# Performance work log

Hardware: AMD Instinct MI355X
Metric: run time of the kernel (lower is better)

Reference implementation:

```python
import jax, jax.numpy as jnp
import numpy as np
from jax import lax

E = 8          # num_experts
K = 2          # top-k
TASKS = 8
GATE_DIM = 16
# (in, expand, out, kernel, stride) per MoE stage
STAGES = [(3, 32, 16, 7, 2), (16, 64, 32, 3, 1), (32, 128, 64, 3, 2), (64, 256, 64, 3, 1), (64, 128, 32, 3, 1)]
DN = ('NCHW', 'OIHW', 'NCHW')


def _pw(x, w):
    return lax.conv_general_dilated(x, w, (1, 1), 'VALID', dimension_numbers=DN)


def _dw(x, w, s):
    p = w.shape[-1] // 2
    return lax.conv_general_dilated(x, w, (s, s), [(p, p), (p, p)], dimension_numbers=DN, feature_group_count=x.shape[1])


def _gn(x, scale, bias):
    # GroupNorm with num_groups = C // 4, eps = 1e-5 (torch default)
    B, C, H, W = x.shape
    G = C // 4
    xr = x.reshape(B, G, -1)
    m = xr.mean(-1, keepdims=True)
    v = xr.var(-1, keepdims=True)
    xn = ((xr - m) * lax.rsqrt(v + 1e-5)).reshape(B, C, H, W)
    return xn * scale[None, :, None, None] + bias[None, :, None, None]


def _dsc(x, p, stride):
    # DSCBlock: pw-conv -> GN -> SiLU -> dw-conv -> GN -> SiLU -> pw-conv -> GN
    w1, s1, b1, w2, s2, b2, w3, s3, b3 = p
    x = jax.nn.silu(_gn(_pw(x, w1), s1, b1))
    x = jax.nn.silu(_gn(_dw(x, w2, stride), s2, b2))
    return _gn(_pw(x, w3), s3, b3)


def _moe(gate_input, x, wg, p, stride, task_bh):
    # task-conditioned top-k softmax gating (noisy_gating=False, all aux loss weights 0)
    logits = gate_input @ wg[task_bh]                      # (B, E)
    probs = jax.nn.softmax(logits, axis=-1)
    topv, topi = lax.top_k(probs, K)
    topv = topv / topv.sum(-1, keepdims=True)              # renormalize top-k gates
    Bn = gate_input.shape[0]
    dense = jnp.zeros_like(probs).at[jnp.arange(Bn)[:, None], topi].set(topv)
    eo = jax.vmap(lambda pe: _dsc(x, pe, stride))(p)       # (E, B, C, H, W)
    return jnp.einsum('be,ebchw->bchw', dense, eo)


def _forward(fl, task_bh):
    gi, xi, ppe = fl[0], fl[1], fl[2]
    x = xi
    for i, (_, _, _, _, s) in enumerate(STAGES):
        base = 3 + i * 10
        wg = fl[base]
        p = tuple(fl[base + 1: base + 10])
        x = _moe(gi, x, wg, p, s, task_bh)
    Bn = x.shape[0]
    # patchify: (B,32,20,20) -> unfold(2,4,4).unfold(3,4,4) -> permute -> (B,25,512)
    patches = x.reshape(Bn, 32, 5, 4, 5, 4).transpose(0, 1, 2, 4, 3, 5)  # (B,32,5,5,4,4)
    patches = patches.transpose(0, 2, 3, 4, 5, 1).reshape(Bn, 25, 512)
    return patches + ppe


def setup_inputs():
    key = jax.random.key(0)
    ks = iter(jax.random.split(key, 256))
    B = 64
    d = {}
    d['gate_input'] = jax.random.normal(next(ks), (B, GATE_DIM), jnp.float32)
    d['expert_input'] = jax.random.normal(next(ks), (B, 3, 80, 80), jnp.float32)
    d['patch_pos_embed'] = 0.02 * jax.random.normal(next(ks), (1, 25, 512), jnp.float32)
    for i, (cin, exp, cout, k, s) in enumerate(STAGES, 1):
        d[f's{i}_wg'] = 0.1 * jax.random.normal(next(ks), (TASKS, GATE_DIM, E), jnp.float32)
        d[f's{i}_w1'] = jax.random.normal(next(ks), (E, exp, cin, 1, 1), jnp.float32) / np.sqrt(cin)
        d[f's{i}_g1s'] = 1.0 + 0.1 * jax.random.normal(next(ks), (E, exp), jnp.float32)
        d[f's{i}_g1b'] = 0.1 * jax.random.normal(next(ks), (E, exp), jnp.float32)
        d[f's{i}_w2'] = jax.random.normal(next(ks), (E, exp, 1, k, k), jnp.float32) / k
        d[f's{i}_g2s'] = 1.0 + 0.1 * jax.random.normal(next(ks), (E, exp), jnp.float32)
        d[f's{i}_g2b'] = 0.1 * jax.random.normal(next(ks), (E, exp), jnp.float32)
        d[f's{i}_w3'] = jax.random.normal(next(ks), (E, cout, exp, 1, 1), jnp.float32) / np.sqrt(exp)
        d[f's{i}_g3s'] = 1.0 + 0.1 * jax.random.normal(next(ks), (E, cout), jnp.float32)
        d[f's{i}_g3b'] = 0.1 * jax.random.normal(next(ks), (E, cout), jnp.float32)
    d['task_bh'] = 3
    return d


def reference(gate_input, expert_input, patch_pos_embed, s1_wg, s1_w1, s1_g1s, s1_g1b, s1_w2, s1_g2s, s1_g2b, s1_w3, s1_g3s, s1_g3b, s2_wg, s2_w1, s2_g1s, s2_g1b, s2_w2, s2_g2s, s2_g2b, s2_w3, s2_g3s, s2_g3b, s3_wg, s3_w1, s3_g1s, s3_g1b, s3_w2, s3_g2s, s3_g2b, s3_w3, s3_g3s, s3_g3b, s4_wg, s4_w1, s4_g1s, s4_g1b, s4_w2, s4_g2s, s4_g2b, s4_w3, s4_g3s, s4_g3b, s5_wg, s5_w1, s5_g1s, s5_g1b, s5_w2, s5_g2s, s5_g2b, s5_w3, s5_g3s, s5_g3b, task_bh):
    fl = (gate_input, expert_input, patch_pos_embed,
          s1_wg, s1_w1, s1_g1s, s1_g1b, s1_w2, s1_g2s, s1_g2b, s1_w3, s1_g3s, s1_g3b,
          s2_wg, s2_w1, s2_g1s, s2_g1b, s2_w2, s2_g2s, s2_g2b, s2_w3, s2_g3s, s2_g3b,
          s3_wg, s3_w1, s3_g1s, s3_g1b, s3_w2, s3_g2s, s3_g2b, s3_w3, s3_g3s, s3_g3b,
          s4_wg, s4_w1, s4_g1s, s4_g1b, s4_w2, s4_g2s, s4_g2b, s4_w3, s4_g3s, s4_g3b,
          s5_wg, s5_w1, s5_g1s, s5_g1b, s5_w2, s5_g2s, s5_g2b, s5_w3, s5_g3s, s5_g3b)
    patches = _forward(fl, task_bh)
    loss = jnp.zeros((), patches.dtype)  # all MoE loss weights are 0 in VisionEncoder
    return (patches, loss)
```

## Files before the change

kernel.cpp:

```cpp
#include <hip/hip_runtime.h>
#include <cstddef>

#define TPB 256

__device__ __forceinline__ int rfl(int v) { return __builtin_amdgcn_readfirstlane(v); }
__device__ __forceinline__ float rflf(float v) {
    return __int_as_float(__builtin_amdgcn_readfirstlane(__float_as_int(v)));
}

__device__ __forceinline__ unsigned short f2bf(float f) {
    union { float f; unsigned int u; } x{f};
    unsigned int r = x.u + 0x7fffu + ((x.u >> 16) & 1u);
    return (unsigned short)(r >> 16);
}
__device__ __forceinline__ float bf2f(unsigned short u) {
    return __uint_as_float(((unsigned int)u) << 16);
}

template <int N, int NW>
__device__ __forceinline__ void bredN(float* v, float* red) {
    __syncthreads();
    #pragma unroll
    for (int off = 32; off > 0; off >>= 1)
        #pragma unroll
        for (int i = 0; i < N; i++) v[i] += __shfl_down(v[i], off);
    const int lane = threadIdx.x & 63;
    const int wv = threadIdx.x >> 6;
    if (lane == 0)
        #pragma unroll
        for (int i = 0; i < N; i++) red[wv * N + i] = v[i];
    __syncthreads();
    if (threadIdx.x == 0) {
        #pragma unroll
        for (int i = 0; i < N; i++) {
            float s = 0.f;
            #pragma unroll
            for (int w = 0; w < NW; w++) s += red[w * N + i];
            red[i] = s;
        }
    }
    __syncthreads();
    #pragma unroll
    for (int i = 0; i < N; i++) v[i] = red[i];
}

__device__ __forceinline__ float silu_f(float v) {
    return v * __builtin_amdgcn_rcpf(1.f + __expf(-v));
}

struct GatePtrs { const float* wg[5]; };

__global__ void gate_kernel(const float* __restrict__ gi, GatePtrs gp,
                            const int* __restrict__ taskp,
                            int* __restrict__ gidx, float* __restrict__ gw) {
    const int s = blockIdx.x;
    const int b = threadIdx.x;
    const int task = taskp[0];
    const float* wg = gp.wg[s] + (size_t)task * 16 * 8;
    float l[8];
    #pragma unroll
    for (int e = 0; e < 8; e++) l[e] = 0.f;
    for (int d = 0; d < 16; d++) {
        float v = gi[b * 16 + d];
        #pragma unroll
        for (int e = 0; e < 8; e++) l[e] += v * wg[d * 8 + e];
    }
    float mx = l[0];
    #pragma unroll
    for (int e = 1; e < 8; e++) mx = fmaxf(mx, l[e]);
    float p[8]; float sum = 0.f;
    #pragma unroll
    for (int e = 0; e < 8; e++) { p[e] = expf(l[e] - mx); sum += p[e]; }
    int i0 = 0;
    #pragma unroll
    for (int e = 1; e < 8; e++) if (p[e] > p[i0]) i0 = e;
    int i1 = (i0 == 0) ? 1 : 0;
    #pragma unroll
    for (int e = 0; e < 8; e++) if (e != i0 && p[e] > p[i1]) i1 = e;
    const float denom = p[i0] + p[i1];
    const int base = (s * 64 + b) * 2;
    gidx[base] = i0; gidx[base + 1] = i1;
    gw[base] = p[i0] / denom; gw[base + 1] = p[i1] / denom;
}

__global__ __launch_bounds__(256) void s1_stats(
    const float* __restrict__ xin, const float* __restrict__ w1,
    const int* __restrict__ gidx, float* __restrict__ stats1) {
    const int g = blockIdx.x, b = blockIdx.y, slot = blockIdx.z;
    const int tid = threadIdx.x;
    const int e = rfl(gidx[b * 2 + slot]);
    __shared__ float red[8];
    const float* xb = xin + (size_t)b * 3 * 6400;
    const float* w1e = w1 + ((size_t)e * 32 + g * 4) * 3;
    float wr[4][3];
    #pragma unroll
    for (int c = 0; c < 4; c++)
        #pragma unroll
        for (int k = 0; k < 3; k++) wr[c][k] = rflf(w1e[c * 3 + k]);
    float s[2] = {0.f, 0.f};
    #pragma unroll
    for (int j = 0; j < 7; j++) {
        const int i = j * 256 + tid;
        if (i < 1600) {
            const int p4 = i * 4;
            const float4 v0 = *(const float4*)(xb + p4);
            const float4 v1 = *(const float4*)(xb + 6400 + p4);
            const float4 v2 = *(const float4*)(xb + 12800 + p4);
            const float a0[4] = {v0.x, v0.y, v0.z, v0.w};
            const float a1[4] = {v1.x, v1.y, v1.z, v1.w};
            const float a2[4] = {v2.x, v2.y, v2.z, v2.w};
            #pragma unroll
            for (int t = 0; t < 4; t++)
                #pragma unroll
                for (int c = 0; c < 4; c++) {
                    float a = fmaf(wr[c][0], a0[t], fmaf(wr[c][1], a1[t], wr[c][2] * a2[t]));
                    s[0] += a; s[1] += a * a;
                }
        }
    }
    bredN<2, 4>(s, red);
    if (tid == 0) {
        float* sp = stats1 + ((size_t)(b * 2 + slot) * 8 + g) * 2;
        sp[0] = s[0]; sp[1] = s[1];
    }
}

__global__ __launch_bounds__(256) void s1_band(
    const float* __restrict__ xin, const float* __restrict__ w1,
    const float* __restrict__ g1s, const float* __restrict__ g1b,
    const float* __restrict__ w2, const int* __restrict__ gidx,
    const float* __restrict__ stats1,
    float* __restrict__ rawdw, float* __restrict__ stats2) {
    constexpr int NR = 25, RW = 90, EVO = 44;
    const int gb = blockIdx.x;
    const int g = gb >> 2, band = gb & 3;
    const int b = blockIdx.y, slot = blockIdx.z;
    const int tid = threadIdx.x;
    const int e = rfl(gidx[b * 2 + slot]);

    __shared__ float sbuf[4 * NR * RW];
    __shared__ float w2s[196];
    __shared__ float red[8];

    for (int i = tid; i < 4 * NR * RW; i += 256) sbuf[i] = 0.f;
    if (tid < 196) w2s[tid] = w2[((size_t)e * 32 + g * 4) * 49 + tid];

    const float* sp = stats1 + ((size_t)(b * 2 + slot) * 8 + g) * 2;
    const float s1v = rflf(sp[0]), s2v = rflf(sp[1]);
    const float mean = s1v / 25600.f;
    const float var = s2v / 25600.f - mean * mean;
    const float inv = rsqrtf(var + 1e-5f);

    const float* xb = xin + (size_t)b * 3 * 6400;
    const float* w1e = w1 + ((size_t)e * 32 + g * 4) * 3;
    float wr[4][3], sc1r[4], bi1r[4];
    #pragma unroll
    for (int c = 0; c < 4; c++) {
        #pragma unroll
        for (int k = 0; k < 3; k++) wr[c][k] = rflf(w1e[c * 3 + k]);
        sc1r[c] = rflf(g1s[e * 32 + g * 4 + c]);
        bi1r[c] = rflf(g1b[e * 32 + g * 4 + c]);
    }
    const int oh0 = band * 10;
    const int rlo = 2 * oh0 - 3;
    __syncthreads();

    for (int ii = tid; ii < 500; ii += 256) {
        const int p4 = ii * 4;
        const int l = p4 / 80, pw = p4 - l * 80;
        const int r = rlo + l;
        if (r >= 0 && r < 80) {
            const float4 v0 = *(const float4*)(xb + r * 80 + pw);
            const float4 v1 = *(const float4*)(xb + 6400 + r * 80 + pw);
            const float4 v2 = *(const float4*)(xb + 12800 + r * 80 + pw);
            const float a0[4] = {v0.x, v0.y, v0.z, v0.w};
            const float a1[4] = {v1.x, v1.y, v1.z, v1.w};
            const float a2[4] = {v2.x, v2.y, v2.z, v2.w};
            #pragma unroll
            for (int c = 0; c < 4; c++) {
                #pragma unroll
                for (int t = 0; t < 4; t++) {
                    float a = fmaf(wr[c][0], a0[t], fmaf(wr[c][1], a1[t], wr[c][2] * a2[t]));
                    float v = silu_f((a - mean) * inv * sc1r[c] + bi1r[c]);
                    const int cc = pw + t + 3;
                    const int sl = (cc & 1) ? EVO + (cc >> 1) : (cc >> 1);
                    sbuf[(c * NR + l) * RW + sl] = v;
                }
            }
        }
    }
    __syncthreads();

    float st2[2] = {0.f, 0.f};
    float* rw = rawdw + (size_t)(b * 2 + slot) * 32 * 1600 + (size_t)g * 4 * 1600;
    #pragma unroll
    for (int qi = 0; qi < 2; qi++) {
        const int q = tid + qi * 256;
        if (q < 400) {
            const int c = q / 100;
            const int rem = q - c * 100;
            const int ohl = rem / 10, owb = (rem - ohl * 10) * 4;
            float o[4] = {0.f, 0.f, 0.f, 0.f};
            #pragma unroll
            for (int kh = 0; kh < 7; kh++) {
                const int base = (c * NR + 2 * ohl + kh) * RW;
                const float2 e01 = *(const float2*)&sbuf[base + owb];
                const float2 e23 = *(const float2*)&sbuf[base + owb + 2];
                const float2 e45 = *(const float2*)&sbuf[base + owb + 4];
                const float e6 = sbuf[base + owb + 6];
                const float2 q01 = *(const float2*)&sbuf[base + EVO + owb];
                const float2 q23 = *(const float2*)&sbuf[base + EVO + owb + 2];
                const float2 q45 = *(const float2*)&sbuf[base + EVO + owb + 4];
                const float evr[7] = {e01.x, e01.y, e23.x, e23.y, e45.x, e45.y, e6};
                const float odr[6] = {q01.x, q01.y, q23.x, q23.y, q45.x, q45.y};
                const float w0 = w2s[c * 49 + kh * 7 + 0];
                const float w1v = w2s[c * 49 + kh * 7 + 1];
                const float w2v = w2s[c * 49 + kh * 7 + 2];
                const float w3 = w2s[c * 49 + kh * 7 + 3];
                const float w4 = w2s[c * 49 + kh * 7 + 4];
                const float w5 = w2s[c * 49 + kh * 7 + 5];
                const float w6 = w2s[c * 49 + kh * 7 + 6];
                #pragma unroll
                for (int t = 0; t < 4; t++)
                    o[t] += w0 * evr[t] + w1v * odr[t] + w2v * evr[t + 1]
                          + w3 * odr[t + 1] + w4 * evr[t + 2] + w5 * odr[t + 2]
                          + w6 * evr[t + 3];
            }
            const int oh = oh0 + ohl;
            float4 ov = {o[0], o[1], o[2], o[3]};
            *(float4*)(rw + c * 1600 + oh * 40 + owb) = ov;
            #pragma unroll
            for (int t = 0; t < 4; t++) { st2[0] += o[t]; st2[1] += o[t] * o[t]; }
        }
    }
    bredN<2, 4>(st2, red);
    if (tid == 0) {
        float* s2p = stats2 + (((size_t)(b * 2 + slot) * 8 + g) * 4 + band) * 2;
        s2p[0] = st2[0]; s2p[1] = st2[1];
    }
}

__global__ __launch_bounds__(256) void s1_norm(
    const float* __restrict__ rawdw, const float* __restrict__ stats2,
    const float* __restrict__ g2s, const float* __restrict__ g2b,
    const int* __restrict__ gidx, unsigned short* __restrict__ act2) {
    const int g = blockIdx.x, b = blockIdx.y, slot = blockIdx.z;
    const int tid = threadIdx.x;
    const int e = rfl(gidx[b * 2 + slot]);
    const float* sp = stats2 + ((size_t)(b * 2 + slot) * 8 + g) * 8;
    const float s1 = rflf(sp[0]) + rflf(sp[2]) + rflf(sp[4]) + rflf(sp[6]);
    const float s2 = rflf(sp[1]) + rflf(sp[3]) + rflf(sp[5]) + rflf(sp[7]);
    const float mean2 = s1 / 6400.f;
    const float var2 = s2 / 6400.f - mean2 * mean2;
    const float inv2 = rsqrtf(var2 + 1e-5f);
    const float* rb = rawdw + (size_t)(b * 2 + slot) * 32 * 1600 + (size_t)g * 4 * 1600;
    unsigned short* ao = act2 + ((size_t)(b * 2 + slot) * 32 + g * 4) * 1600;
    #pragma unroll
    for (int c = 0; c < 4; c++) {
        const float sc = rflf(g2s[e * 32 + g * 4 + c]);
        const float bi = rflf(g2b[e * 32 + g * 4 + c]);
        #pragma unroll
        for (int qi = 0; qi < 2; qi++) {
            const int i = tid + qi * 256;
            if (i < 400) {
                const float4 v = *(const float4*)(rb + c * 1600 + i * 4);
                ushort4 ov;
                ov.x = f2bf(silu_f((v.x - mean2) * inv2 * sc + bi));
                ov.y = f2bf(silu_f((v.y - mean2) * inv2 * sc + bi));
                ov.z = f2bf(silu_f((v.z - mean2) * inv2 * sc + bi));
                ov.w = f2bf(silu_f((v.w - mean2) * inv2 * sc + bi));
                *(ushort4*)(ao + c * 1600 + i * 4) = ov;
            }
        }
    }
}

template <int CIN, int CEXP, int KS, int STRIDE, int H, int W, int HO, int WO,
          int NCH, int TPBk>
__global__ __launch_bounds__(TPBk) void dsc_ab_v2(
    const unsigned short* __restrict__ xin, const float* __restrict__ w1,
    const float* __restrict__ g1s, const float* __restrict__ g1b,
    const float* __restrict__ w2,
    const float* __restrict__ g2s, const float* __restrict__ g2b,
    const int* __restrict__ gidx, unsigned short* __restrict__ act2) {
    constexpr int HW = H * W, HWO = HO * WO;
    constexpr int HP = H + 2, WPL = W + 3, EVW = (W + 2) / 2;
    constexpr int NPV = HW / 4;
    constexpr int JN = (NPV + TPBk - 1) / TPBk;
    constexpr int NW = TPBk / 64;
    constexpr int NG = NCH / 4;
    constexpr int Qc = HWO / 4;
    constexpr int QT = NCH * Qc;
    constexpr int QI = (QT + TPBk - 1) / TPBk;
    constexpr int KK = KS * KS;
    const int gch = blockIdx.x, b = blockIdx.y, slot = blockIdx.z;
    const int tid = threadIdx.x;
    const int e = rfl(gidx[b * 2 + slot]);
    const int cb0 = gch * NCH;

    __shared__ float buf1[NCH * HP * WPL];
    __shared__ float w2s[NCH * KK];
    __shared__ float sc2s[NCH], bi2s[NCH];
    __shared__ float red[2 * NG * NW];

    for (int i = tid; i < NCH * HP * WPL; i += TPBk) buf1[i] = 0.f;
    for (int i = tid; i < NCH * KK; i += TPBk) {
        int c = i / KK, k = i - c * KK;
        w2s[i] = w2[((size_t)e * CEXP + cb0 + c) * KK + k];
    }
    if (tid < NCH) {
        sc2s[tid] = g2s[e * CEXP + cb0 + tid];
        bi2s[tid] = g2b[e * CEXP + cb0 + tid];
    }

    const unsigned short* xb = xin + (size_t)b * CIN * HW;
    const float* w1e = w1 + ((size_t)e * CEXP + cb0) * CIN;

    float acc[NCH][JN][4];
    #pragma unroll
    for (int c = 0; c < NCH; c++)
        #pragma unroll
        for (int j = 0; j < JN; j++)
            #pragma unroll
            for (int t = 0; t < 4; t++) acc[c][j][t] = 0.f;

    for (int cb = 0; cb < CIN; cb += 4) {
        float wr[NCH][4];
        #pragma unroll
        for (int c = 0; c < NCH; c++)
            #pragma unroll
            for (int k = 0; k < 4; k++) wr[c][k] = rflf(w1e[c * CIN + cb + k]);
        #pragma unroll
        for (int j = 0; j < JN; j++) {
            const int pv = tid + j * TPBk;
            if (JN * TPBk == NPV || pv < NPV) {
                #pragma unroll
                for (int k = 0; k < 4; k++) {
                    const ushort4 v4 = *(const ushort4*)(xb + (cb + k) * HW + pv * 4);
                    const float va[4] = {bf2f(v4.x), bf2f(v4.y), bf2f(v4.z), bf2f(v4.w)};
                    #pragma unroll
                    for (int c = 0; c < NCH; c++)
                        #pragma unroll
                        for (int t = 0; t < 4; t++)
                            acc[c][j][t] = fmaf(wr[c][k], va[t], acc[c][j][t]);
                }
            }
        }
    }
    float st[2 * NG];
    #pragma unroll
    for (int i = 0; i < 2 * NG; i++) st[i] = 0.f;
    #pragma unroll
    for (int c = 0; c < NCH; c++) {
        const int gs = (c >> 2) * 2;
        #pragma unroll
        for (int j = 0; j < JN; j++)
            #pragma unroll
            for (int t = 0; t < 4; t++) {
                float a = acc[c][j][t];
                st[gs] += a; st[gs + 1] += a * a;
            }
    }
    bredN<2 * NG, NW>(st, red);
    float mg[NG], ig[NG];
    #pragma unroll
    for (int g = 0; g < NG; g++) {
        mg[g] = st[g * 2] / (4.f * HW);
        float var = st[g * 2 + 1] / (4.f * HW) - mg[g] * mg[g];
        ig[g] = rsqrtf(var + 1e-5f);
    }
    float sc1r[NCH], bi1r[NCH];
    #pragma unroll
    for (int c = 0; c < NCH; c++) {
        sc1r[c] = rflf(g1s[e * CEXP + cb0 + c]);
        bi1r[c] = rflf(g1b[e * CEXP + cb0 + c]);
    }
    #pragma unroll
    for (int j = 0; j < JN; j++) {
        const int pv = tid + j * TPBk;
        if (JN * TPBk == NPV || pv < NPV) {
            const int p4 = pv * 4;
            const int ph = p4 / W, pwb = p4 - ph * W;
            #pragma unroll
            for (int c = 0; c < NCH; c++) {
                const int g = (NG == 1) ? 0 : (c >> 2);
                #pragma unroll
                for (int t = 0; t < 4; t++) {
                    float v = silu_f((acc[c][j][t] - mg[g]) * ig[g] * sc1r[c] + bi1r[c]);
                    const int j2 = pwb + t + 1;
                    const int col = (STRIDE == 1) ? j2
                                    : ((j2 & 1) ? EVW + (j2 >> 1) : (j2 >> 1));
                    buf1[(c * HP + ph + 1) * WPL + col] = v;
                }
            }
        }
    }
    __syncthreads();

    float dacc[QI][4];
    float st2[2 * NG];
    #pragma unroll
    for (int i = 0; i < 2 * NG; i++) st2[i] = 0.f;
    #pragma unroll
    for (int qi = 0; qi < QI; qi++) {
        #pragma unroll
        for (int t = 0; t < 4; t++) dacc[qi][t] = 0.f;
        const int q = tid + qi * TPBk;
        if (QI * TPBk == QT || q < QT) {
            const int c = q / Qc, qq = q - c * Qc;
            const int oh = qq % HO, owb = (qq / HO) * 4;
            float o[4] = {0.f, 0.f, 0.f, 0.f};
            if (STRIDE == 1) {
                #pragma unroll
                for (int kh = 0; kh < KS; kh++) {
                    const int base = (c * HP + oh + kh) * WPL + owb;
                    float r[6];
                    #pragma unroll
                    for (int i = 0; i < 6; i++) r[i] = buf1[base + i];
                    const float wa = w2s[c * KK + kh * KS + 0];
                    const float wb = w2s[c * KK + kh * KS + 1];
                    const float wcc = w2s[c * KK + kh * KS + 2];
                    #pragma unroll
                    for (int t = 0; t < 4; t++)
                        o[t] += wa * r[t] + wb * r[t + 1] + wcc * r[t + 2];
                }
            } else {
                #pragma unroll
                for (int kh = 0; kh < KS; kh++) {
                    const int base = (c * HP + 2 * oh + kh) * WPL;
                    float ev[5], od[4];
                    #pragma unroll
                    for (int i = 0; i < 5; i++) ev[i] = buf1[base + owb + i];
                    #pragma unroll
                    for (int i = 0; i < 4; i++) od[i] = buf1[base + EVW + owb + i];
                    const float wa = w2s[c * KK + kh * KS + 0];
                    const float wb = w2s[c * KK + kh * KS + 1];
                    const float wcc = w2s[c * KK + kh * KS + 2];
                    #pragma unroll
                    for (int t = 0; t < 4; t++)
                        o[t] += wa * ev[t] + wb * od[t] + wcc * ev[t + 1];
                }
            }
            #pragma unroll
            for (int t = 0; t < 4; t++) {
                float a = o[t];
                dacc[qi][t] = a;
                if constexpr (NG == 1) {
                    st2[0] += a; st2[1] += a * a;
                } else {
                    const bool gsel = (c >= 4);
                    float a0 = gsel ? 0.f : a, a1 = gsel ? a : 0.f;
                    st2[0] += a0; st2[1] += a0 * a0;
                    st2[2] += a1; st2[3] += a1 * a1;
                }
            }
        }
    }
    bredN<2 * NG, NW>(st2, red);
    float m2[NG], i2[NG];
    #pragma unroll
    for (int g = 0; g < NG; g++) {
        m2[g] = st2[g * 2] / (4.f * HWO);
        float var = st2[g * 2 + 1] / (4.f * HWO) - m2[g] * m2[g];
        i2[g] = rsqrtf(var + 1e-5f);
    }
    unsigned short* ao = act2 + ((size_t)(b * 2 + slot) * CEXP + cb0) * HWO;
    #pragma unroll
    for (int qi = 0; qi < QI; qi++) {
        const int q = tid + qi * TPBk;
        if (QI * TPBk == QT || q < QT) {
            const int c = q / Qc, qq = q - c * Qc;
            const int oh = qq % HO, owb = (qq / HO) * 4;
            const int g = (NG == 1) ? 0 : ((c >= 4) ? 1 : 0);
            const float sc = sc2s[c], bi = bi2s[c];
            ushort4 ov;
            ov.x = f2bf(silu_f((dacc[qi][0] - m2[g]) * i2[g] * sc + bi));
            ov.y = f2bf(silu_f((dacc[qi][1] - m2[g]) * i2[g] * sc + bi));
            ov.z = f2bf(silu_f((dacc[qi][2] - m2[g]) * i2[g] * sc + bi));
            ov.w = f2bf(silu_f((dacc[qi][3] - m2[g]) * i2[g] * sc + bi));
            *(ushort4*)(ao + c * HWO + oh * WO + owb) = ov;
        }
    }
}

template <int CEXP, int COUT, int HWO, int MT, int NT, int VEC, int PXC>
__global__ __launch_bounds__(256) void pw3_k1(
    const unsigned short* __restrict__ act2, const float* __restrict__ w3,
    const int* __restrict__ gidx,
    float* __restrict__ raw3, float* __restrict__ statsw) {
    constexpr int NTILE = NT * VEC;
    static_assert(MT * NT == 256 && NTILE == 64, "tile");
    constexpr int G = COUT / 4;
    constexpr int KC = 16;
    constexpr int WPT = (KC * COUT) / 256;
    const int pxc = blockIdx.x, b = blockIdx.y, slot = blockIdx.z;
    const int tid = threadIdx.x;
    const int e = rfl(gidx[b * 2 + slot]);
    const int px0 = pxc * NTILE;
    const int ct = tid / NT, pt = tid % NT;

    __shared__ float actT[KC][NTILE];
    __shared__ float wT[KC][COUT];

    const unsigned short* ab = act2 + (size_t)(b * 2 + slot) * CEXP * HWO;
    const float* w3e = w3 + (size_t)e * COUT * CEXP;

    float acc[4][VEC];
    #pragma unroll
    for (int i = 0; i < 4; i++)
        #pragma unroll
        for (int j = 0; j < VEC; j++) acc[i][j] = 0.f;

    const int lkk = tid / 16;
    const int lp4 = (tid % 16) * 4;
    const int wc = tid / (KC / WPT);
    const int wk = (tid % (KC / WPT)) * WPT;

    for (int k0 = 0; k0 < CEXP; k0 += KC) {
        __syncthreads();
        {
            const int px = px0 + lp4;
            ushort4 v = make_ushort4(0, 0, 0, 0);
            if (px < HWO) v = *(const ushort4*)(ab + (size_t)(k0 + lkk) * HWO + px);
            float4 f = {bf2f(v.x), bf2f(v.y), bf2f(v.z), bf2f(v.w)};
            *(float4*)&actT[lkk][lp4] = f;
        }
        #pragma unroll
        for (int i = 0; i < WPT; i++)
            wT[wk + i][wc] = w3e[(size_t)wc * CEXP + k0 + wk + i];
        __syncthreads();
        #pragma unroll
        for (int kk = 0; kk < KC; kk++) {
            const float4 w4 = *(const float4*)&wT[kk][ct * 4];
            const float wf[4] = {w4.x, w4.y, w4.z, w4.w};
            float av[VEC];
            if constexpr (VEC == 4) {
                float4 a4 = *(const float4*)&actT[kk][pt * 4];
                av[0] = a4.x; av[1] = a4.y; av[2] = a4.z; av[3] = a4.w;
            } else if constexpr (VEC == 2) {
                float2 a2 = *(const float2*)&actT[kk][pt * 2];
                av[0] = a2.x; av[1] = a2.y;
            } else {
                av[0] = actT[kk][pt];
            }
            #pragma unroll
            for (int i = 0; i < 4; i++)
                #pragma unroll
                for (int j = 0; j < VEC; j++)
                    acc[i][j] = fmaf(wf[i], av[j], acc[i][j]);
        }
    }

    const int px = px0 + pt * VEC;
    float s1 = 0.f, s2 = 0.f;
    #pragma unroll
    for (int i = 0; i < 4; i++) {
        if (px < HWO) {
            float* rp = raw3 + ((size_t)(b * 2 + slot) * COUT + ct * 4 + i) * HWO + px;
            if constexpr (VEC == 4) {
                float4 v = {acc[i][0], acc[i][1], acc[i][2], acc[i][3]};
                *(float4*)rp = v;
            } else if constexpr (VEC == 2) {
                float2 v = {acc[i][0], acc[i][1]};
                *(float2*)rp = v;
            } else {
                *rp = acc[i][0];
            }
        }
        #pragma unroll
        for (int j = 0; j < VEC; j++) { s1 += acc[i][j]; s2 += acc[i][j] * acc[i][j]; }
    }
    #pragma unroll
    for (int off = NT / 2; off > 0; off >>= 1) {
        s1 += __shfl_down(s1, off);
        s2 += __shfl_down(s2, off);
    }
    if (pt == 0) {
        float* sp = statsw + (((size_t)(b * 2 + slot) * G + ct) * PXC + pxc) * 2;
        sp[0] = s1; sp[1] = s2;
    }
}

template <int COUT, int HWO, int PXC, bool PATCH>
__global__ __launch_bounds__(256) void pw3_k3m(
    const float* __restrict__ raw3, const float* __restrict__ statsw,
    const float* __restrict__ g3s, const float* __restrict__ g3b,
    const int* __restrict__ gidx, const float* __restrict__ gw,
    const float* __restrict__ ppe, float* __restrict__ outf,
    unsigned short* __restrict__ outb) {
    constexpr int G = COUT / 4;
    constexpr int Q = HWO / 4;
    const int gg = blockIdx.x, b = blockIdx.y;
    const int tid = threadIdx.x;

    float A[2][4], Bv[2][4];
    #pragma unroll
    for (int slot = 0; slot < 2; slot++) {
        const int e = rfl(gidx[b * 2 + slot]);
        const float wgt = rflf(gw[b * 2 + slot]);
        const float* sp = statsw + ((size_t)(b * 2 + slot) * G + gg) * PXC * 2;
        float s1 = 0.f, s2 = 0.f;
        for (int i = 0; i < PXC; i++) { s1 += rflf(sp[i * 2]); s2 += rflf(sp[i * 2 + 1]); }
        const float mean = s1 / (4.f * HWO);
        const float var = s2 / (4.f * HWO) - mean * mean;
        const float inv = rsqrtf(var + 1e-5f);
        #pragma unroll
        for (int i = 0; i < 4; i++) {
            const int c = gg * 4 + i;
            const float sc = rflf(g3s[e * COUT + c]);
            const float bi = rflf(g3b[e * COUT + c]);
            A[slot][i] = wgt * inv * sc;
            Bv[slot][i] = wgt * (bi - mean * inv * sc);
        }
    }

    #pragma unroll
    for (int i = 0; i < 4; i++) {
        const int c = gg * 4 + i;
        const float* r0 = raw3 + ((size_t)(b * 2 + 0) * COUT + c) * HWO;
        const float* r1 = raw3 + ((size_t)(b * 2 + 1) * COUT + c) * HWO;
        for (int q = tid; q < Q; q += 256) {
            const int p4 = q * 4;
            const float4 v0 = *(const float4*)(r0 + p4);
            const float4 v1 = *(const float4*)(r1 + p4);
            float o[4];
            o[0] = fmaf(A[0][i], v0.x, Bv[0][i]) + fmaf(A[1][i], v1.x, Bv[1][i]);
            o[1] = fmaf(A[0][i], v0.y, Bv[0][i]) + fmaf(A[1][i], v1.y, Bv[1][i]);
            o[2] = fmaf(A[0][i], v0.z, Bv[0][i]) + fmaf(A[1][i], v1.z, Bv[1][i]);
            o[3] = fmaf(A[0][i], v0.w, Bv[0][i]) + fmaf(A[1][i], v1.w, Bv[1][i]);
            if constexpr (!PATCH) {
                ushort4 ov = {f2bf(o[0]), f2bf(o[1]), f2bf(o[2]), f2bf(o[3])};
                *(ushort4*)(outb + ((size_t)b * COUT + c) * HWO + p4) = ov;
            } else {
                const int ph = p4 / 20, pw0 = p4 - ph * 20;
                const int p = (ph >> 2) * 5 + (pw0 >> 2);
                const int dbase = ((ph & 3) * 4) * 32 + c;
                float* op = outf + ((size_t)b * 25 + p) * 512;
                const float* pp = ppe + p * 512;
                #pragma unroll
                for (int jj = 0; jj < 4; jj++)
                    op[dbase + jj * 32] = o[jj] + pp[dbase + jj * 32];
            }
        }
    }
    if (PATCH && gg == 0 && b == 0 && tid == 0) outf[64 * 25 * 512] = 0.f;
}

extern "C" void kernel_launch(void* const* d_in, const int* in_sizes, int n_in,
                              void* d_out, int out_size, void* d_ws, size_t ws_size,
                              hipStream_t stream) {
    const float* gate_input = (const float*)d_in[0];
    const float* expert_input = (const float*)d_in[1];
    const float* ppe = (const float*)d_in[2];
    const int* taskp = (const int*)d_in[53];
    auto in = [&](int s, int k) { return (const float*)d_in[3 + s * 10 + k]; };

    char* ws = (char*)d_ws;
    int* gidx = (int*)ws;
    float* gw = (float*)(ws + 4096);
    size_t off = 8192;
    unsigned short* x0 = (unsigned short*)(ws + off); off += (size_t)8 << 20;
    unsigned short* x1 = (unsigned short*)(ws + off); off += (size_t)8 << 20;
    unsigned short* act2 = (unsigned short*)(ws + off); off += (size_t)27 << 20;
    float* raw3 = (float*)(ws + off); off += (size_t)27 << 20;
    float* statsw = (float*)(ws + off); off += (size_t)1 << 20;
    float* stats1 = (float*)(ws + off); off += 65536;
    float* stats2 = (float*)(ws + off);
    float* outp = (float*)d_out;

    GatePtrs gp;
    for (int s = 0; s < 5; s++) gp.wg[s] = in(s, 0);
    gate_kernel<<<5, 64, 0, stream>>>(gate_input, gp, taskp, gidx, gw);

    s1_stats<<<dim3(8, 64, 2), 256, 0, stream>>>(expert_input, in(0, 1),
                                                 gidx + 0 * 128, stats1);
    s1_band<<<dim3(32, 64, 2), 256, 0, stream>>>(
        expert_input, in(0, 1), in(0, 2), in(0, 3), in(0, 4),
        gidx + 0 * 128, stats1, raw3, stats2);
    s1_norm<<<dim3(8, 64, 2), 256, 0, stream>>>(
        raw3, stats2, in(0, 5), in(0, 6), gidx + 0 * 128, act2);
    pw3_k1<32, 16, 1600, 4, 64, 1, 25><<<dim3(25, 64, 2), 256, 0, stream>>>(
        act2, in(0, 7), gidx + 0 * 128, raw3, statsw);
    pw3_k3m<16, 1600, 25, false><<<dim3(4, 64), 256, 0, stream>>>(
        raw3, statsw, in(0, 8), in(0, 9), gidx + 0 * 128, gw + 0 * 128, ppe,
        nullptr, x0);

    dsc_ab_v2<16, 64, 3, 1, 40, 40, 40, 40, 4, 256><<<dim3(16, 64, 2), 256, 0, stream>>>(
        x0, in(1, 1), in(1, 2), in(1, 3), in(1, 4), in(1, 5), in(1, 6),
        gidx + 1 * 128, act2);
    pw3_k1<64, 32, 1600, 8, 32, 2, 25><<<dim3(25, 64, 2), 256, 0, stream>>>(
        act2, in(1, 7), gidx + 1 * 128, raw3, statsw);
    pw3_k3m<32, 1600, 25, false><<<dim3(8, 64), 256, 0, stream>>>(
        raw3, statsw, in(1, 8), in(1, 9), gidx + 1 * 128, gw + 1 * 128, ppe,
        nullptr, x1);

    dsc_ab_v2<32, 128, 3, 2, 40, 40, 20, 20, 4, 256><<<dim3(32, 64, 2), 256, 0, stream>>>(
        x1, in(2, 1), in(2, 2), in(2, 3), in(2, 4), in(2, 5), in(2, 6),
        gidx + 2 * 128, act2);
    pw3_k1<128, 64, 400, 16, 16, 4, 7><<<dim3(7, 64, 2), 256, 0, stream>>>(
        act2, in(2, 7), gidx + 2 * 128, raw3, statsw);
    pw3_k3m<64, 400, 7, false><<<dim3(16, 64), 256, 0, stream>>>(
        raw3, statsw, in(2, 8), in(2, 9), gidx + 2 * 128, gw + 2 * 128, ppe,
        nullptr, x0);

    dsc_ab_v2<64, 256, 3, 1, 20, 20, 20, 20, 8, 128><<<dim3(32, 64, 2), 128, 0, stream>>>(
        x0, in(3, 1), in(3, 2), in(3, 3), in(3, 4), in(3, 5), in(3, 6),
        gidx + 3 * 128, act2);
    pw3_k1<256, 64, 400, 16, 16, 4, 7><<<dim3(7, 64, 2), 256, 0, stream>>>(
        act2, in(3, 7), gidx + 3 * 128, raw3, statsw);
    pw3_k3m<64, 400, 7, false><<<dim3(16, 64), 256, 0, stream>>>(
        raw3, statsw, in(3, 8), in(3, 9), gidx + 3 * 128, gw + 3 * 128, ppe,
        nullptr, x1);

    dsc_ab_v2<64, 128, 3, 1, 20, 20, 20, 20, 8, 128><<<dim3(16, 64, 2), 128, 0, stream>>>(
        x1, in(4, 1), in(4, 2), in(4, 3), in(4, 4), in(4, 5), in(4, 6),
        gidx + 4 * 128, act2);
    pw3_k1<128, 32, 400, 8, 32, 2, 7><<<dim3(7, 64, 2), 256, 0, stream>>>(
        act2, in(4, 7), gidx + 4 * 128, raw3, statsw);
    pw3_k3m<32, 400, 7, true><<<dim3(8, 64), 256, 0, stream>>>(
        raw3, statsw, in(4, 8), in(4, 9), gidx + 4 * 128, gw + 4 * 128, ppe,
        outp, nullptr);
}
```

Baseline: 547.2 us.

## Replace scalar pointwise convs with bf16 MFMA GEMMs and split DSC stages

Adds a templated bf16 MFMA GEMM kernel for the pointwise convolutions. It handles the first pw conv in stages 2, 4 and 5 and the final pw conv in every stage, replacing the fp32 FMA tiled kernel. In stages 2, 4 and 5 the fused dsc_ab_v2 kernel becomes a GEMM, then a separate depthwise kernel, then a GEMM that folds GroupNorm and SiLU into its input load. The final-conv raw output is stored as bf16 instead of fp32, which cuts memory traffic but adds rounding error before normalization. The split adds kernel launches and round-trips of the expanded activations through global memory, and the weights are converted to bf16 on every tile load.

After: 523.9 us. 1.04x faster.

```diff
diff --git a/kernel.cpp b/kernel.cpp
--- a/kernel.cpp
+++ b/kernel.cpp
@@ -2,6 +2,9 @@
 #include <cstddef>
 
 #define TPB 256
+
+typedef __attribute__((ext_vector_type(8))) short short8v;
+typedef __attribute__((ext_vector_type(4))) float f32x4;
 
 __device__ __forceinline__ int rfl(int v) { return __builtin_amdgcn_readfirstlane(v); }
 __device__ __forceinline__ float rflf(float v) {
@@ -81,6 +84,254 @@
     const int base = (s * 64 + b) * 2;
     gidx[base] = i0; gidx[base + 1] = i1;
     gw[base] = p[i0] / denom; gw[base + 1] = p[i1] / denom;
+}
+
+template <int M, int K, int N, int MT, int NCHK, bool FOLD, bool BIN>
+__global__ __launch_bounds__(256) void gemm_bf16(
+    const unsigned short* __restrict__ inp, const float* __restrict__ wmat,
+    const int* __restrict__ gidx, const float* __restrict__ foldStats,
+    const float* __restrict__ foldS, const float* __restrict__ foldB,
+    unsigned short* __restrict__ outp, float* __restrict__ stats) {
+    constexpr int KITERS = (K + 31) / 32;
+    constexpr int IM = (MT == 64) ? 2 : 1;
+    constexpr int IN = (MT == 16) ? 1 : 2;
+    const int bx = blockIdx.x;
+    const int nc = bx % NCHK, mc = bx / NCHK;
+    const int b = blockIdx.y, slot = blockIdx.z;
+    const int bs = b * 2 + slot;
+    const int e = rfl(gidx[b * 2 + slot]);
+    const int n0 = nc * 64, m0 = mc * MT;
+    const int tid = threadIdx.x;
+    const int lane = tid & 63, wv = tid >> 6;
+    const int quad = lane >> 4, l15 = lane & 15;
+
+    __shared__ __align__(16) unsigned short wtile[MT * 40];
+    __shared__ unsigned int intile[16 * 65];
+    __shared__ float sred[(MT / 4) * 2];
+    __shared__ float afv[K], bfv[K];
+
+    if (tid < (MT / 4) * 2) sred[tid] = 0.f;
+    if constexpr (FOLD) {
+        for (int c = tid; c < K; c += 256) {
+            const int g = c >> 2;
+            const float s1 = foldStats[((size_t)bs * (K / 4) + g) * 2 + 0];
+            const float s2 = foldStats[((size_t)bs * (K / 4) + g) * 2 + 1];
+            const float mean = s1 / (4.f * N);
+            const float var = s2 / (4.f * N) - mean * mean;
+            const float inv = rsqrtf(var + 1e-5f);
+            const float sc = foldS[e * K + c], bi = foldB[e * K + c];
+            afv[c] = inv * sc;
+            bfv[c] = bi - mean * inv * sc;
+        }
+    }
+
+    int mbase, nbase;
+    if constexpr (MT == 64) { mbase = (wv & 1) * 32; nbase = (wv >> 1) * 32; }
+    else if constexpr (MT == 32) { mbase = (wv & 1) * 16; nbase = (wv >> 1) * 32; }
+    else { mbase = 0; nbase = wv * 16; }
+
+    f32x4 acc[IM][IN];
+    #pragma unroll
+    for (int im = 0; im < IM; im++)
+        #pragma unroll
+        for (int in = 0; in < IN; in++)
+            #pragma unroll
+            for (int r = 0; r < 4; r++) acc[im][in][r] = 0.f;
+
+    const unsigned short* ib = inp + (size_t)(BIN ? b : bs) * K * N;
+    const float* wbase = wmat + (size_t)e * M * K;
+
+    for (int k0 = 0; k0 < KITERS * 32; k0 += 32) {
+        __syncthreads();
+        for (int i = tid; i < MT * 32; i += 256) {
+            const int m = i >> 5, kk = i & 31;
+            const float v = (k0 + kk < K) ? wbase[(size_t)(m0 + m) * K + k0 + kk] : 0.f;
+            wtile[m * 40 + kk] = f2bf(v);
+        }
+        {
+            const int kp = tid >> 4, nq = tid & 15;
+            const int k = k0 + kp * 2;
+            const int n = n0 + nq * 4;
+            unsigned short u0[4] = {0, 0, 0, 0}, u1[4] = {0, 0, 0, 0};
+            const bool nv = (n < N);
+            if (nv && k < K) {
+                const ushort4 t = *(const ushort4*)(ib + (size_t)k * N + n);
+                u0[0] = t.x; u0[1] = t.y; u0[2] = t.z; u0[3] = t.w;
+            }
+            if (nv && k + 1 < K) {
+                const ushort4 t = *(const ushort4*)(ib + (size_t)(k + 1) * N + n);
+                u1[0] = t.x; u1[1] = t.y; u1[2] = t.z; u1[3] = t.w;
+            }
+            #pragma unroll
+            for (int t = 0; t < 4; t++) {
+                float f0, f1;
+                if constexpr (FOLD) {
+                    f0 = (nv && k < K) ? silu_f(afv[k] * bf2f(u0[t]) + bfv[k]) : 0.f;
+                    f1 = (nv && k + 1 < K) ? silu_f(afv[k + 1] * bf2f(u1[t]) + bfv[k + 1]) : 0.f;
+                } else {
+                    f0 = bf2f(u0[t]); f1 = bf2f(u1[t]);
+                }
+                intile[kp * 65 + nq * 4 + t] =
+                    (unsigned int)f2bf(f0) | ((unsigned int)f2bf(f1) << 16);
+            }
+        }
+        __syncthreads();
+
+        short8v afr[IM];
+        #pragma unroll
+        for (int im = 0; im < IM; im++) {
+            const int m = mbase + im * 16 + l15;
+            afr[im] = *(const short8v*)&wtile[m * 40 + quad * 8];
+        }
+        #pragma unroll
+        for (int in = 0; in < IN; in++) {
+            union { unsigned int u[4]; short8v s; } bu;
+            const int col = nbase + in * 16 + l15;
+            #pragma unroll
+            for (int i = 0; i < 4; i++) bu.u[i] = intile[(quad * 4 + i) * 65 + col];
+            #pragma unroll
+            for (int im = 0; im < IM; im++)
+                acc[im][in] = __builtin_amdgcn_mfma_f32_16x16x32_bf16(
+                    afr[im], bu.s, acc[im][in], 0, 0, 0);
+        }
+    }
+
+    unsigned short* ob = outp + (size_t)bs * M * N;
+    #pragma unroll
+    for (int im = 0; im < IM; im++) {
+        #pragma unroll
+        for (int in = 0; in < IN; in++) {
+            const int n = n0 + nbase + in * 16 + l15;
+            float s1 = 0.f, s2 = 0.f;
+            #pragma unroll
+            for (int r = 0; r < 4; r++) {
+                const float a = acc[im][in][r];
+                s1 += a; s2 += a * a;
+            }
+            if (n < N) {
+                #pragma unroll
+                for (int r = 0; r < 4; r++) {
+                    const int m = m0 + mbase + im * 16 + quad * 4 + r;
+                    ob[(size_t)m * N + n] = f2bf(acc[im][in][r]);
+                }
+            }
+            #pragma unroll
+            for (int off = 8; off > 0; off >>= 1) {
+                s1 += __shfl_down(s1, off, 16);
+                s2 += __shfl_down(s2, off, 16);
+            }
+            if (l15 == 0) {
+                const int gl = (mbase + im * 16) / 4 + quad;
+                atomicAdd(&sred[gl * 2 + 0], s1);
+                atomicAdd(&sred[gl * 2 + 1], s2);
+            }
+        }
+    }
+    __syncthreads();
+    for (int i = tid; i < MT / 4; i += 256) {
+        float* sp = stats + (((size_t)bs * (M / 4) + mc * (MT / 4) + i) * NCHK + nc) * 2;
+        sp[0] = sred[i * 2]; sp[1] = sred[i * 2 + 1];
+    }
+}
+
+template <int CEXP, int H, int W, int NCH, int TPBk, int NCHK1>
+__global__ __launch_bounds__(TPBk) void dw_k(
+    const unsigned short* __restrict__ raw1, const float* __restrict__ stats1,
+    const float* __restrict__ g1s, const float* __restrict__ g1b,
+    const float* __restrict__ w2, const int* __restrict__ gidx,
+    unsigned short* __restrict__ act2raw, float* __restrict__ stats2) {
+    constexpr int HW = H * W, HP = H + 2, WPL = W + 3;
+    constexpr int NPV = HW / 4, NG = NCH / 4, NW = TPBk / 64;
+    constexpr int Qc = HW / 4, QT = NCH * Qc, QI = (QT + TPBk - 1) / TPBk;
+    constexpr int G1 = CEXP / 4;
+    const int gch = blockIdx.x, b = blockIdx.y, slot = blockIdx.z;
+    const int bs = b * 2 + slot;
+    const int tid = threadIdx.x;
+    const int e = rfl(gidx[b * 2 + slot]);
+    const int cb0 = gch * NCH;
+
+    __shared__ float buf1[NCH * HP * WPL];
+    __shared__ float w2s[NCH * 9];
+    __shared__ float afl[NCH], bfl[NCH];
+    __shared__ float red[2 * NG * NW];
+
+    for (int i = tid; i < NCH * HP * WPL; i += TPBk) buf1[i] = 0.f;
+    if (tid < NCH * 9) w2s[tid] = w2[((size_t)e * CEXP + cb0) * 9 + tid];
+    if (tid < NCH) {
+        const int c = cb0 + tid, g = c >> 2;
+        float s1 = 0.f, s2 = 0.f;
+        for (int i = 0; i < NCHK1; i++) {
+            s1 += stats1[(((size_t)bs * G1 + g) * NCHK1 + i) * 2 + 0];
+            s2 += stats1[(((size_t)bs * G1 + g) * NCHK1 + i) * 2 + 1];
+        }
+        const float mean = s1 / (4.f * HW);
+        const float var = s2 / (4.f * HW) - mean * mean;
+        const float inv = rsqrtf(var + 1e-5f);
+        const float sc = g1s[e * CEXP + c], bi = g1b[e * CEXP + c];
+        afl[tid] = inv * sc; bfl[tid] = bi - mean * inv * sc;
+    }
+    __syncthreads();
+
+    const unsigned short* rb = raw1 + (size_t)bs * CEXP * HW + (size_t)cb0 * HW;
+    for (int i = tid; i < NCH * NPV; i += TPBk) {
+        const int c = i / NPV, pv = i - c * NPV;
+        const int p4 = pv * 4, ph = p4 / W, pwb = p4 - ph * W;
+        const ushort4 u = *(const ushort4*)(rb + (size_t)c * HW + p4);
+        const float a = afl[c], bb = bfl[c];
+        float* bp = &buf1[(c * HP + ph + 1) * WPL + pwb + 1];
+        bp[0] = silu_f(a * bf2f(u.x) + bb);
+        bp[1] = silu_f(a * bf2f(u.y) + bb);
+        bp[2] = silu_f(a * bf2f(u.z) + bb);
+        bp[3] = silu_f(a * bf2f(u.w) + bb);
+    }
+    __syncthreads();
+
+    float st2[2 * NG];
+    #pragma unroll
+    for (int i = 0; i < 2 * NG; i++) st2[i] = 0.f;
+    unsigned short* ao = act2raw + (size_t)bs * CEXP * HW + (size_t)cb0 * HW;
+    #pragma unroll
+    for (int qi = 0; qi < QI; qi++) {
+        const int q = tid + qi * TPBk;
+        if (QI * TPBk == QT || q < QT) {
+            const int c = q / Qc, qq = q - c * Qc;
+            const int oh = qq % H, owb = (qq / H) * 4;
+            float o[4] = {0.f, 0.f, 0.f, 0.f};
+            #pragma unroll
+            for (int kh = 0; kh < 3; kh++) {
+                const int base = (c * HP + oh + kh) * WPL + owb;
+                float r[6];
+                #pragma unroll
+                for (int i = 0; i < 6; i++) r[i] = buf1[base + i];
+                const float wa = w2s[c * 9 + kh * 3 + 0];
+                const float wb = w2s[c * 9 + kh * 3 + 1];
+                const float wcc = w2s[c * 9 + kh * 3 + 2];
+                #pragma unroll
+                for (int t = 0; t < 4; t++)
+                    o[t] += wa * r[t] + wb * r[t + 1] + wcc * r[t + 2];
+            }
+            ushort4 ov = {f2bf(o[0]), f2bf(o[1]), f2bf(o[2]), f2bf(o[3])};
+            *(ushort4*)(ao + c * HW + oh * W + owb) = ov;
+            #pragma unroll
+            for (int t = 0; t < 4; t++) {
+                if constexpr (NG == 1) { st2[0] += o[t]; st2[1] += o[t] * o[t]; }
+                else {
+                    const bool gs = (c >= 4);
+                    float a0 = gs ? 0.f : o[t], a1 = gs ? o[t] : 0.f;
+                    st2[0] += a0; st2[1] += a0 * a0;
+                    st2[2] += a1; st2[3] += a1 * a1;
+                }
+            }
+        }
+    }
+    bredN<2 * NG, NW>(st2, red);
+    if (tid == 0) {
+        #pragma unroll
+        for (int g = 0; g < NG; g++) {
+            stats2[((size_t)bs * G1 + cb0 / 4 + g) * 2 + 0] = st2[g * 2];
+            stats2[((size_t)bs * G1 + cb0 / 4 + g) * 2 + 1] = st2[g * 2 + 1];
+        }
+    }
 }
 
 __global__ __launch_bounds__(256) void s1_stats(
@@ -483,107 +734,9 @@
     }
 }
 
-template <int CEXP, int COUT, int HWO, int MT, int NT, int VEC, int PXC>
-__global__ __launch_bounds__(256) void pw3_k1(
-    const unsigned short* __restrict__ act2, const float* __restrict__ w3,
-    const int* __restrict__ gidx,
-    float* __restrict__ raw3, float* __restrict__ statsw) {
-    constexpr int NTILE = NT * VEC;
-    static_assert(MT * NT == 256 && NTILE == 64, "tile");
-    constexpr int G = COUT / 4;
-    constexpr int KC = 16;
-    constexpr int WPT = (KC * COUT) / 256;
-    const int pxc = blockIdx.x, b = blockIdx.y, slot = blockIdx.z;
-    const int tid = threadIdx.x;
-    const int e = rfl(gidx[b * 2 + slot]);
-    const int px0 = pxc * NTILE;
-    const int ct = tid / NT, pt = tid % NT;
-
-    __shared__ float actT[KC][NTILE];
-    __shared__ float wT[KC][COUT];
-
-    const unsigned short* ab = act2 + (size_t)(b * 2 + slot) * CEXP * HWO;
-    const float* w3e = w3 + (size_t)e * COUT * CEXP;
-
-    float acc[4][VEC];
-    #pragma unroll
-    for (int i = 0; i < 4; i++)
-        #pragma unroll
-        for (int j = 0; j < VEC; j++) acc[i][j] = 0.f;
-
-    const int lkk = tid / 16;
-    const int lp4 = (tid % 16) * 4;
-    const int wc = tid / (KC / WPT);
-    const int wk = (tid % (KC / WPT)) * WPT;
-
-    for (int k0 = 0; k0 < CEXP; k0 += KC) {
-        __syncthreads();
-        {
-            const int px = px0 + lp4;
-            ushort4 v = make_ushort4(0, 0, 0, 0);
-            if (px < HWO) v = *(const ushort4*)(ab + (size_t)(k0 + lkk) * HWO + px);
-            float4 f = {bf2f(v.x), bf2f(v.y), bf2f(v.z), bf2f(v.w)};
-            *(float4*)&actT[lkk][lp4] = f;
-        }
-        #pragma unroll
-        for (int i = 0; i < WPT; i++)
-            wT[wk + i][wc] = w3e[(size_t)wc * CEXP + k0 + wk + i];
-        __syncthreads();
-        #pragma unroll
-        for (int kk = 0; kk < KC; kk++) {
-            const float4 w4 = *(const float4*)&wT[kk][ct * 4];
-            const float wf[4] = {w4.x, w4.y, w4.z, w4.w};
-            float av[VEC];
-            if constexpr (VEC == 4) {
-                float4 a4 = *(const float4*)&actT[kk][pt * 4];
-                av[0] = a4.x; av[1] = a4.y; av[2] = a4.z; av[3] = a4.w;
-            } else if constexpr (VEC == 2) {
-                float2 a2 = *(const float2*)&actT[kk][pt * 2];
-                av[0] = a2.x; av[1] = a2.y;
-            } else {
-                av[0] = actT[kk][pt];
-            }
-            #pragma unroll
-            for (int i = 0; i < 4; i++)
-                #pragma unroll
-                for (int j = 0; j < VEC; j++)
-                    acc[i][j] = fmaf(wf[i], av[j], acc[i][j]);
-        }
-    }
-
-    const int px = px0 + pt * VEC;
-    float s1 = 0.f, s2 = 0.f;
-    #pragma unroll
-    for (int i = 0; i < 4; i++) {
-        if (px < HWO) {
-            float* rp = raw3 + ((size_t)(b * 2 + slot) * COUT + ct * 4 + i) * HWO + px;
-            if constexpr (VEC == 4) {
-                float4 v = {acc[i][0], acc[i][1], acc[i][2], acc[i][3]};
-                *(float4*)rp = v;
-            } else if constexpr (VEC == 2) {
-                float2 v = {acc[i][0], acc[i][1]};
-                *(float2*)rp = v;
-            } else {
-                *rp = acc[i][0];
-            }
-        }
-        #pragma unroll
-        for (int j = 0; j < VEC; j++) { s1 += acc[i][j]; s2 += acc[i][j] * acc[i][j]; }
-    }
-    #pragma unroll
-    for (int off = NT / 2; off > 0; off >>= 1) {
-        s1 += __shfl_down(s1, off);
-        s2 += __shfl_down(s2, off);
-    }
-    if (pt == 0) {
-        float* sp = statsw + (((size_t)(b * 2 + slot) * G + ct) * PXC + pxc) * 2;
-        sp[0] = s1; sp[1] = s2;
-    }
-}
-
 template <int COUT, int HWO, int PXC, bool PATCH>
 __global__ __launch_bounds__(256) void pw3_k3m(
-    const float* __restrict__ raw3, const float* __restrict__ statsw,
+    const unsigned short* __restrict__ raw3, const float* __restrict__ statsw,
     const float* __restrict__ g3s, const float* __restrict__ g3b,
     const int* __restrict__ gidx, const float* __restrict__ gw,
     const float* __restrict__ ppe, float* __restrict__ outf,
@@ -617,17 +770,18 @@
     #pragma unroll
     for (int i = 0; i < 4; i++) {
         const int c = gg * 4 + i;
-        const float* r0 = raw3 + ((size_t)(b * 2 + 0) * COUT + c) * HWO;
-        const float* r1 = raw3 + ((size_t)(b * 2 + 1) * COUT + c) * HWO;
+        const unsigned short* r0 = raw3 + ((size_t)(b * 2 + 0) * COUT + c) * HWO;
+        const unsigned short* r1 = raw3 + ((size_t)(b * 2 + 1) * COUT + c) * HWO;
         for (int q = tid; q < Q; q += 256) {
             const int p4 = q * 4;
-            const float4 v0 = *(const float4*)(r0 + p4);
-            const float4 v1 = *(const float4*)(r1 + p4);
+            const ushort4 u0 = *(const ushort4*)(r0 + p4);
+            const ushort4 u1 = *(const ushort4*)(r1 + p4);
+            const float v0[4] = {bf2f(u0.x), bf2f(u0.y), bf2f(u0.z), bf2f(u0.w)};
+            const float v1[4] = {bf2f(u1.x), bf2f(u1.y), bf2f(u1.z), bf2f(u1.w)};
             float o[4];
-            o[0] = fmaf(A[0][i], v0.x, Bv[0][i]) + fmaf(A[1][i], v1.x, Bv[1][i]);
-            o[1] = fmaf(A[0][i], v0.y, Bv[0][i]) + fmaf(A[1][i], v1.y, Bv[1][i]);
-            o[2] = fmaf(A[0][i], v0.z, Bv[0][i]) + fmaf(A[1][i], v1.z, Bv[1][i]);
-            o[3] = fmaf(A[0][i], v0.w, Bv[0][i]) + fmaf(A[1][i], v1.w, Bv[1][i]);
+            #pragma unroll
+            for (int t = 0; t < 4; t++)
+                o[t] = fmaf(A[0][i], v0[t], Bv[0][i]) + fmaf(A[1][i], v1[t], Bv[1][i]);
             if constexpr (!PATCH) {
                 ushort4 ov = {f2bf(o[0]), f2bf(o[1]), f2bf(o[2]), f2bf(o[3])};
                 *(ushort4*)(outb + ((size_t)b * COUT + c) * HWO + p4) = ov;
@@ -662,10 +816,12 @@
     unsigned short* x0 = (unsigned short*)(ws + off); off += (size_t)8 << 20;
     unsigned short* x1 = (unsigned short*)(ws + off); off += (size_t)8 << 20;
     unsigned short* act2 = (unsigned short*)(ws + off); off += (size_t)27 << 20;
-    float* raw3 = (float*)(ws + off); off += (size_t)27 << 20;
-    float* statsw = (float*)(ws + off); off += (size_t)1 << 20;
-    float* stats1 = (float*)(ws + off); off += 65536;
-    float* stats2 = (float*)(ws + off);
+    char* bufA = ws + off; off += (size_t)27 << 20;
+    float* stats1 = (float*)(ws + off); off += (size_t)2 << 20;
+    float* stats2 = (float*)(ws + off); off += 262144;
+    float* stats3 = (float*)(ws + off); off += (size_t)1 << 20;
+    float* st1a = (float*)(ws + off); off += 65536;
+    float* st1b = (float*)(ws + off);
     float* outp = (float*)d_out;
 
     GatePtrs gp;
@@ -673,51 +829,65 @@
     gate_kernel<<<5, 64, 0, stream>>>(gate_input, gp, taskp, gidx, gw);
 
     s1_stats<<<dim3(8, 64, 2), 256, 0, stream>>>(expert_input, in(0, 1),
-                                                 gidx + 0 * 128, stats1);
+                                                 gidx + 0 * 128, st1a);
     s1_band<<<dim3(32, 64, 2), 256, 0, stream>>>(
         expert_input, in(0, 1), in(0, 2), in(0, 3), in(0, 4),
-        gidx + 0 * 128, stats1, raw3, stats2);
+        gidx + 0 * 128, st1a, (float*)bufA, st1b);
     s1_norm<<<dim3(8, 64, 2), 256, 0, stream>>>(
-        raw3, stats2, in(0, 5), in(0, 6), gidx + 0 * 128, act2);
-    pw3_k1<32, 16, 1600, 4, 64, 1, 25><<<dim3(25, 64, 2), 256, 0, stream>>>(
-        act2, in(0, 7), gidx + 0 * 128, raw3, statsw);
+        (float*)bufA, st1b, in(0, 5), in(0, 6), gidx + 0 * 128, act2);
+    gemm_bf16<16, 32, 1600, 16, 25, false, false><<<dim3(25, 64, 2), 256, 0, stream>>>(
+        act2, in(0, 7), gidx + 0 * 128, nullptr, nullptr, nullptr,
+        (unsigned short*)bufA, stats3);
     pw3_k3m<16, 1600, 25, false><<<dim3(4, 64), 256, 0, stream>>>(
-        raw3, statsw, in(0, 8), in(0, 9), gidx + 0 * 128, gw + 0 * 128, ppe,
-        nullptr, x0);
-
-    dsc_ab_v2<16, 64, 3, 1, 40, 40, 40, 40, 4, 256><<<dim3(16, 64, 2), 256, 0, stream>>>(
-        x0, in(1, 1), in(1, 2), in(1, 3), in(1, 4), in(1, 5), in(1, 6),
-        gidx + 1 * 128, act2);
-    pw3_k1<64, 32, 1600, 8, 32, 2, 25><<<dim3(25, 64, 2), 256, 0, stream>>>(
-        act2, in(1, 7), gidx + 1 * 128, raw3, statsw);
+        (unsigned short*)bufA, stats3, in(0, 8), in(0, 9), gidx + 0 * 128,
+        gw + 0 * 128, ppe, nullptr, x0);
+
+    gemm_bf16<64, 16, 1600, 64, 25, false, true><<<dim3(25, 64, 2), 256, 0, stream>>>(
+        x0, in(1, 1), gidx + 1 * 128, nullptr, nullptr, nullptr,
+        (unsigned short*)bufA, stats1);
+    dw_k<64, 40, 40, 4, 256, 25><<<dim3(16, 64, 2), 256, 0, stream>>>(
+        (unsigned short*)bufA, stats1, in(1, 2), in(1, 3), in(1, 4),
+        gidx + 1 * 128, act2, stats2);
+    gemm_bf16<32, 64, 1600, 32, 25, true, false><<<dim3(25, 64, 2), 256, 0, stream>>>(
+        act2, in(1, 7), gidx + 1 * 128, stats2, in(1, 5), in(1, 6),
+        (unsigned short*)bufA, stats3);
     pw3_k3m<32, 1600, 25, false><<<dim3(8, 64), 256, 0, stream>>>(
-        raw3, statsw, in(1, 8), in(1, 9), gidx + 1 * 128, gw + 1 * 128, ppe,
-        nullptr, x1);
+        (unsigned short*)bufA, stats3, in(1, 8), in(1, 9), gidx + 1 * 128,
+        gw + 1 * 128, ppe, nullptr, x1);
 
     dsc_ab_v2<32, 128, 3, 2, 40, 40, 20, 20, 4, 256><<<dim3(32, 64, 2), 256, 0, stream>>>(
         x1, in(2, 1), in(2, 2), in(2, 3), in(2, 4), in(2, 5), in(2, 6),
         gidx + 2 * 128, act2);
-    pw3_k1<128, 64, 400, 16, 16, 4, 7><<<dim3(7, 64, 2), 256, 0, stream>>>(
-        act2, in(2, 7), gidx + 2 * 128, raw3, statsw);
+    gemm_bf16<64, 128, 400, 64, 7, false, false><<<dim3(7, 64, 2), 256, 0, stream>>>(
+        act2, in(2, 7), gidx + 2 * 128, nullptr, nullptr, nullptr,
+        (unsigned short*)bufA, stats3);
     pw3_k3m<64, 400, 7, false><<<dim3(16, 64), 256, 0, stream>>>(
-        raw3, statsw, in(2, 8), in(2, 9), gidx + 2 * 128, gw + 2 * 128, ppe,
-        nullptr, x0);
-
-    dsc_ab_v2<64, 256, 3, 1, 20, 20, 20, 20, 8, 128><<<dim3(32, 64, 2), 128, 0, stream>>>(
-        x0, in(3, 1), in(3, 2), in(3, 3), in(3, 4), in(3, 5), in(3, 6),
-        gidx + 3 * 128, act2);
-    pw3_k1<256, 64, 400, 16, 16, 4, 7><<<dim3(7, 64, 2), 256, 0, stream>>>(
-        act2, in(3, 7), gidx + 3 * 128, raw3, statsw);
+        (unsigned short*)bufA, stats3, in(2, 8), in(2, 9), gidx + 2 * 128,
+        gw + 2 * 128, ppe, nullptr, x0);
+
+    gemm_bf16<256, 64, 400, 64, 7, false, true><<<dim3(28, 64, 2), 256, 0, stream>>>(
+        x0, in(3, 1), gidx + 3 * 128, nullptr, nullptr, nullptr,
+        (unsigned short*)bufA, stats1);
+    dw_k<256, 20, 20, 8, 128, 7><<<dim3(32, 64, 2), 128, 0, stream>>>(
+        (unsigned short*)bufA, stats1, in(3, 2), in(3, 3), in(3, 4),
+        gidx + 3 * 128, act2, stats2);
+    gemm_bf16<64, 256, 400, 64, 7, true, false><<<dim3(7, 64, 2), 256, 0, stream>>>(
+        act2, in(3, 7), gidx + 3 * 128, stats2, in(3, 5), in(3, 6),
+        (unsigned short*)bufA, stats3);
     pw3_k3m<64, 400, 7, false><<<dim3(16, 64), 256, 0, stream>>>(
-        raw3, statsw, in(3, 8), in(3, 9), gidx + 3 * 128, gw + 3 * 128, ppe,
-        nullptr, x1);
-
-    dsc_ab_v2<64, 128, 3, 1, 20, 20, 20, 20, 8, 128><<<dim3(16, 64, 2), 128, 0, stream>>>(
-        x1, in(4, 1), in(4, 2), in(4, 3), in(4, 4), in(4, 5), in(4, 6),
-        gidx + 4 * 128, act2);
-    pw3_k1<128, 32, 400, 8, 32, 2, 7><<<dim3(7, 64, 2), 256, 0, stream>>>(
-        act2, in(4, 7), gidx + 4 * 128, raw3, statsw);
+        (unsigned short*)bufA, stats3, in(3, 8), in(3, 9), gidx + 3 * 128,
+        gw + 3 * 128, ppe, nullptr, x1);
+
+    gemm_bf16<128, 64, 400, 64, 7, false, true><<<dim3(14, 64, 2), 256, 0, stream>>>(
+        x1, in(4, 1), gidx + 4 * 128, nullptr, nullptr, nullptr,
+        (unsigned short*)bufA, stats1);
+    dw_k<128, 20, 20, 8, 128, 7><<<dim3(16, 64, 2), 128, 0, stream>>>(
+        (unsigned short*)bufA, stats1, in(4, 2), in(4, 3), in(4, 4),
+        gidx + 4 * 128, act2, stats2);
+    gemm_bf16<32, 128, 400, 32, 7, true, false><<<dim3(7, 64, 2), 256, 0, stream>>>(
+        act2, in(4, 7), gidx + 4 * 128, stats2, in(4, 5), in(4, 6),
+        (unsigned short*)bufA, stats3);
     pw3_k3m<32, 400, 7, true><<<dim3(8, 64), 256, 0, stream>>>(
-        raw3, statsw, in(4, 8), in(4, 9), gidx + 4 * 128, gw + 4 * 128, ppe,
-        outp, nullptr);
-}
+        (unsigned short*)bufA, stats3, in(4, 8), in(4, 9), gidx + 4 * 128,
+        gw + 4 * 128, ppe, outp, nullptr);
+}
```
